# Optimization experiments

Measured on AMD Instinct MI355X. Metric: run time of the kernel, lower is better.

Reference implementation:

```python
import jax, jax.numpy as jnp
import numpy as np

B, S, E, H = 2, 2048, 1024, 16
D = E // H  # head_dim = 64
FE = 4      # forward_expansion
EPS = 1e-5


def layernorm(x, g, b):
    mu = jnp.mean(x, axis=-1, keepdims=True)
    var = jnp.var(x, axis=-1, keepdims=True)
    return (x - mu) * jax.lax.rsqrt(var + EPS) * g + b


def setup_inputs() -> dict:
    key = jax.random.key(0)
    ks = jax.random.split(key, 16)
    s = lambda d: 1.0 / np.sqrt(d)
    return {
        "queries": jax.random.normal(ks[0], (B, S, E), jnp.float32),
        "keys": jax.random.normal(ks[1], (B, S, E), jnp.float32),
        "values": jax.random.normal(ks[2], (B, S, E), jnp.float32),
        "mask": jnp.ones((B, 1, S, S), jnp.int32),  # ignored (faithful to source bug)
        "Wq": jax.random.normal(ks[3], (D, D), jnp.float32) * s(D),
        "Wk": jax.random.normal(ks[4], (D, D), jnp.float32) * s(D),
        "Wv": jax.random.normal(ks[5], (D, D), jnp.float32) * s(D),
        "Wfc": jax.random.normal(ks[6], (E, E), jnp.float32) * s(E),
        "bfc": jnp.zeros((E,), jnp.float32),
        "W1": jax.random.normal(ks[7], (FE * E, E), jnp.float32) * s(E),
        "b1": jnp.zeros((FE * E,), jnp.float32),
        "W2": jax.random.normal(ks[8], (E, FE * E), jnp.float32) * s(FE * E),
        "b2": jnp.zeros((E,), jnp.float32),
        "ln1_g": jnp.ones((E,), jnp.float32),
        "ln1_b": jnp.zeros((E,), jnp.float32),
        "ln2_g": jnp.ones((E,), jnp.float32),
        "ln2_b": jnp.zeros((E,), jnp.float32),
    }


def reference(queries, keys, values, mask, Wq, Wk, Wv, Wfc, bfc, W1, b1, W2, b2,
              ln1_g, ln1_b, ln2_g, ln2_b):
    # --- MHA ---
    q = queries.reshape(B, S, H, D) @ Wq.T  # [B,S,H,D]
    k = keys.reshape(B, S, H, D) @ Wk.T
    v = values.reshape(B, S, H, D) @ Wv.T
    scores = jnp.einsum('bqhd,bkhd->bhqk', q, k)
    # source: softmax(scores / S**(-1/2)) == scores * sqrt(S)  (faithful quirk)
    # mask is ignored: source masked_fill is non-inplace and discarded
    attn = jax.nn.softmax(scores * jnp.sqrt(jnp.float32(S)), axis=-1)
    out = jnp.einsum('bhqk,bkhd->bqhd', attn, v).reshape(B, S, E)
    att = out @ Wfc.T + bfc
    # --- residual + LN + FFN + LN (dropout p=0 -> identity) ---
    h = layernorm(att + queries, ln1_g, ln1_b)
    x = jax.nn.relu(h @ W1.T + b1) @ W2.T + b2
    return layernorm(x + h, ln2_g, ln2_b)
```

## Files before the change

kernel.cpp:

```cpp
#include <hip/hip_runtime.h>
#include <hip/hip_bf16.h>
#include <math.h>

#define B_ 2
#define S_ 2048
#define E_ 1024
#define H_ 16
#define D_ 64
#define TOK (B_*S_)
#define SCALE 45.254833995939045f
#define SCALE2 (45.254833995939045f * 1.44269504088896340f)

typedef __bf16 bf16x8 __attribute__((ext_vector_type(8)));
typedef float floatx4 __attribute__((ext_vector_type(4)));
struct b4s { __hip_bfloat16 x, y, z, w; };

typedef const __attribute__((address_space(1))) char ga_char;
typedef __attribute__((address_space(3))) char ls_char;

__device__ __forceinline__ void gload_lds16(const void* g, ls_char* l) {
  __builtin_amdgcn_global_load_lds((ga_char*)g, l, 16, 0, 0);
}

#if __has_builtin(__builtin_amdgcn_exp2f)
#define EXP2(x) __builtin_amdgcn_exp2f(x)
#else
#define EXP2(x) exp2f(x)
#endif

#define SWZ(arr, half, row, qpos) \
  (*(bf16x8*)&arr[half][row][(((qpos) ^ ((row) & 3)) * 8)])

__device__ __forceinline__ int fsw(int r) {
  return ((r >> 3) & 1) | ((((r >> 4) ^ (r >> 2)) & 1) << 1);
}
#define SWZ2(arr, half, row, qpos) \
  (*(bf16x8*)&arr[half][row][(((qpos) ^ fsw(row)) * 8)])

__global__ __launch_bounds__(256) void cast_all(
    const float* __restrict__ Wfc, const float* __restrict__ W1,
    const float* __restrict__ W2, __hip_bfloat16* __restrict__ Wfcb,
    __hip_bfloat16* __restrict__ W1b, __hip_bfloat16* __restrict__ W2b,
    const float* __restrict__ Wq, const float* __restrict__ Wk,
    const float* __restrict__ Wv, __hip_bfloat16* __restrict__ Whl) {
  const int i = blockIdx.x * 256 + threadIdx.x;
  if (i < 2359296) {
    const float* src; __hip_bfloat16* dst; int j;
    if (i < 262144)       { src = Wfc; dst = Wfcb; j = i; }
    else if (i < 1310720) { src = W1;  dst = W1b;  j = i - 262144; }
    else                  { src = W2;  dst = W2b;  j = i - 1310720; }
    float4 v = ((const float4*)src)[j];
    b4s o;
    o.x = __float2bfloat16(v.x); o.y = __float2bfloat16(v.y);
    o.z = __float2bfloat16(v.z); o.w = __float2bfloat16(v.w);
    *(b4s*)(dst + (size_t)j * 4) = o;
  } else if (i < 2362368) {
    const int idx = i - 2359296;
    const int m = idx >> 10;
    const int off = (idx & 1023) * 4;
    const float* W = (m == 0) ? Wq : (m == 1) ? Wk : Wv;
    float4 v = *(const float4*)(W + off);
    b4s hi, lo;
    hi.x = __float2bfloat16(v.x); lo.x = __float2bfloat16(v.x - __bfloat162float(hi.x));
    hi.y = __float2bfloat16(v.y); lo.y = __float2bfloat16(v.y - __bfloat162float(hi.y));
    hi.z = __float2bfloat16(v.z); lo.z = __float2bfloat16(v.z - __bfloat162float(hi.z));
    hi.w = __float2bfloat16(v.w); lo.w = __float2bfloat16(v.w - __bfloat162float(hi.w));
    *(b4s*)(Whl + (size_t)m * 8192 + off) = hi;
    *(b4s*)(Whl + (size_t)m * 8192 + 4096 + off) = lo;
  }
}

__global__ __launch_bounds__(256) void qkv_fused(
    const float* __restrict__ xq, const float* __restrict__ xk,
    const float* __restrict__ xv, const __hip_bfloat16* __restrict__ Whl,
    __hip_bfloat16* __restrict__ qhi, __hip_bfloat16* __restrict__ qlo,
    __hip_bfloat16* __restrict__ khi, __hip_bfloat16* __restrict__ klo,
    __hip_bfloat16* __restrict__ vt) {
  __shared__ __bf16 Xh[2][64][32], Xl[2][64][32];
  __shared__ __bf16 Vt[64][72];
  const int t = threadIdx.x, lane = t & 63, w = t >> 6;
  const int quad = lane >> 4, low = lane & 15;
  const int bh = blockIdx.y;
  const int b = bh >> 4, h = bh & 15;
  const int s0 = blockIdx.x * 64;
  const int sr = t >> 2;
  const int sc = (t & 3) * 16;
  const int scc = sc >> 5;
  const int p0 = (sc & 31) >> 3;

  for (int m = 0; m < 3; m++) {
    const float* xin = (m == 0) ? xq : (m == 1) ? xk : xv;
    const __hip_bfloat16* Wh = Whl + (size_t)m * 8192;
    const float sc_m = (m == 0) ? SCALE2 : 1.0f;

    __syncthreads();
    {
      const float* src = xin + ((size_t)(b * S_ + s0 + sr)) * E_ + h * 64 + sc;
      float4 f0 = *(const float4*)(src);
      float4 f1 = *(const float4*)(src + 4);
      float4 f2 = *(const float4*)(src + 8);
      float4 f3 = *(const float4*)(src + 12);
      float fv[16] = {f0.x, f0.y, f0.z, f0.w, f1.x, f1.y, f1.z, f1.w,
                      f2.x, f2.y, f2.z, f2.w, f3.x, f3.y, f3.z, f3.w};
      bf16x8 hi0, hi1, lo0, lo1;
      #pragma unroll
      for (int j = 0; j < 8; j++) {
        hi0[j] = (__bf16)fv[j];
        lo0[j] = (__bf16)(fv[j] - (float)hi0[j]);
        hi1[j] = (__bf16)fv[8 + j];
        lo1[j] = (__bf16)(fv[8 + j] - (float)hi1[j]);
      }
      SWZ(Xh, scc, sr, p0) = hi0;
      SWZ(Xh, scc, sr, p0 + 1) = hi1;
      SWZ(Xl, scc, sr, p0) = lo0;
      SWZ(Xl, scc, sr, p0 + 1) = lo1;
    }
    __syncthreads();

    bf16x8 ah[2], al[2];
    #pragma unroll
    for (int c = 0; c < 2; c++) {
      ah[c] = SWZ(Xh, c, w * 16 + low, quad);
      al[c] = SWZ(Xl, c, w * 16 + low, quad);
    }

    floatx4 acc[4];
    #pragma unroll
    for (int nn = 0; nn < 4; nn++) {
      floatx4 a = {};
      #pragma unroll
      for (int c = 0; c < 2; c++) {
        const __hip_bfloat16* wp = Wh + (nn * 16 + low) * 64 + c * 32 + quad * 8;
        bf16x8 wh_ = *(const bf16x8*)wp;
        bf16x8 wl_ = *(const bf16x8*)(wp + 4096);
        a = __builtin_amdgcn_mfma_f32_16x16x32_bf16(ah[c], wh_, a, 0, 0, 0);
        a = __builtin_amdgcn_mfma_f32_16x16x32_bf16(al[c], wh_, a, 0, 0, 0);
        a = __builtin_amdgcn_mfma_f32_16x16x32_bf16(ah[c], wl_, a, 0, 0, 0);
      }
      acc[nn] = a;
    }

    if (m < 2) {
      __hip_bfloat16* dh = (m == 0) ? qhi : khi;
      __hip_bfloat16* dl = (m == 0) ? qlo : klo;
      #pragma unroll
      for (int nn = 0; nn < 4; nn++) {
        #pragma unroll
        for (int i = 0; i < 4; i++) {
          const int s = s0 + w * 16 + quad * 4 + i;
          const int d = nn * 16 + low;
          const size_t adr = ((size_t)bh * S_ + s) * 64 + d;
          const float f = acc[nn][i] * sc_m;
          const __hip_bfloat16 hb = __float2bfloat16(f);
          dh[adr] = hb;
          dl[adr] = __float2bfloat16(f - __bfloat162float(hb));
        }
      }
    } else {
      #pragma unroll
      for (int nn = 0; nn < 4; nn++)
        #pragma unroll
        for (int i = 0; i < 4; i++)
          Vt[nn * 16 + low][w * 16 + quad * 4 + i] = (__bf16)acc[nn][i];
      __syncthreads();
      const int dr = t >> 2;
      const int scl = (t & 3) * 16;
      __hip_bfloat16* dst = vt + ((size_t)bh * 64 + dr) * S_ + s0 + scl;
      bf16x8 o0 = *(const bf16x8*)&Vt[dr][scl];
      bf16x8 o1 = *(const bf16x8*)&Vt[dr][scl + 8];
      *(bf16x8*)dst = o0;
      *(bf16x8*)(dst + 8) = o1;
    }
  }
}

__global__ __launch_bounds__(512, 4) void attn_mfma(
    const __hip_bfloat16* __restrict__ Qhi, const __hip_bfloat16* __restrict__ Qlo,
    const __hip_bfloat16* __restrict__ Khi, const __hip_bfloat16* __restrict__ Klo,
    const __hip_bfloat16* __restrict__ Vtg, __hip_bfloat16* __restrict__ ctx) {
  __shared__ __bf16 Kh[2][2][64][32], Kl[2][2][64][32], Vs[2][2][64][32];
  const int t = threadIdx.x, lane = t & 63, w = t >> 6;
  const int quad = lane >> 4, low = lane & 15;
  const int bh = blockIdx.x;
  const int qw = blockIdx.y * 128 + w * 16;

  const int sh = w >> 2;
  const int r0 = (w & 3) * 16;
  const int srow = r0 + (lane >> 2);
  const int sq = (lane & 3) ^ fsw(srow);
  const __hip_bfloat16* gK = Khi + ((size_t)bh * S_ + srow) * 64 + sh * 32 + sq * 8;
  const __hip_bfloat16* gL = Klo + ((size_t)bh * S_ + srow) * 64 + sh * 32 + sq * 8;
  const __hip_bfloat16* gV = Vtg + ((size_t)bh * 64 + srow) * S_ + sh * 32 + sq * 8;

  bf16x8 qh[2], ql[2];
  {
    const size_t qbase = ((size_t)bh * S_ + qw + low) * 64 + quad * 8;
    qh[0] = *(const bf16x8*)(Qhi + qbase);
    qh[1] = *(const bf16x8*)(Qhi + qbase + 32);
    ql[0] = *(const bf16x8*)(Qlo + qbase);
    ql[1] = *(const bf16x8*)(Qlo + qbase + 32);
  }

  floatx4 oacc[4] = {};
  float mrow = -3e38f, lrow = 0.f;

  gload_lds16(gK, (ls_char*)&Kh[0][sh][r0][0]);
  gload_lds16(gL, (ls_char*)&Kl[0][sh][r0][0]);
  gload_lds16(gV, (ls_char*)&Vs[0][sh][r0][0]);

  for (int kt = 0; kt < S_ / 64; kt++) {
    const int cur = kt & 1;
    __syncthreads();
    if (kt + 1 < S_ / 64) {
      gload_lds16(gK + (size_t)(kt + 1) * 4096, (ls_char*)&Kh[cur ^ 1][sh][r0][0]);
      gload_lds16(gL + (size_t)(kt + 1) * 4096, (ls_char*)&Kl[cur ^ 1][sh][r0][0]);
      gload_lds16(gV + (size_t)(kt + 1) * 64,   (ls_char*)&Vs[cur ^ 1][sh][r0][0]);
    }

    floatx4 sa[4];
    #pragma unroll
    for (int nn = 0; nn < 4; nn++) {
      const int prow = (nn & 1) * 32 + (nn >> 1) * 4 + (low >> 2) * 8 + (low & 3);
      bf16x8 kh0 = SWZ2(Kh[cur], 0, prow, quad);
      bf16x8 kh1 = SWZ2(Kh[cur], 1, prow, quad);
      bf16x8 kl0 = SWZ2(Kl[cur], 0, prow, quad);
      bf16x8 kl1 = SWZ2(Kl[cur], 1, prow, quad);
      floatx4 s = {};
      s = __builtin_amdgcn_mfma_f32_16x16x32_bf16(kh0, qh[0], s, 0, 0, 0);
      s = __builtin_amdgcn_mfma_f32_16x16x32_bf16(kh1, qh[1], s, 0, 0, 0);
      s = __builtin_amdgcn_mfma_f32_16x16x32_bf16(kl0, qh[0], s, 0, 0, 0);
      s = __builtin_amdgcn_mfma_f32_16x16x32_bf16(kl1, qh[1], s, 0, 0, 0);
      s = __builtin_amdgcn_mfma_f32_16x16x32_bf16(kh0, ql[0], s, 0, 0, 0);
      s = __builtin_amdgcn_mfma_f32_16x16x32_bf16(kh1, ql[1], s, 0, 0, 0);
      sa[nn] = s;
    }

    float rmax;
    {
      float m0 = fmaxf(fmaxf(sa[0][0], sa[0][1]), fmaxf(sa[0][2], sa[0][3]));
      float m1 = fmaxf(fmaxf(sa[1][0], sa[1][1]), fmaxf(sa[1][2], sa[1][3]));
      float m2 = fmaxf(fmaxf(sa[2][0], sa[2][1]), fmaxf(sa[2][2], sa[2][3]));
      float m3 = fmaxf(fmaxf(sa[3][0], sa[3][1]), fmaxf(sa[3][2], sa[3][3]));
      rmax = fmaxf(fmaxf(m0, m1), fmaxf(m2, m3));
      rmax = fmaxf(rmax, __shfl_xor(rmax, 16, 64));
      rmax = fmaxf(rmax, __shfl_xor(rmax, 32, 64));
    }
    if (__any(rmax > mrow)) {
      const float nm = fmaxf(mrow, rmax);
      const float al = EXP2(mrow - nm);
      mrow = nm;
      lrow *= al;
      #pragma unroll
      for (int dt = 0; dt < 4; dt++) {
        oacc[dt][0] *= al; oacc[dt][1] *= al;
        oacc[dt][2] *= al; oacc[dt][3] *= al;
      }
    }
    float p[4][4];
    float rs;
    {
      float r0_ = 0.f, r1_ = 0.f, r2_ = 0.f, r3_ = 0.f;
      #pragma unroll
      for (int i = 0; i < 4; i++) {
        p[0][i] = EXP2(sa[0][i] - mrow); r0_ += p[0][i];
        p[1][i] = EXP2(sa[1][i] - mrow); r1_ += p[1][i];
        p[2][i] = EXP2(sa[2][i] - mrow); r2_ += p[2][i];
        p[3][i] = EXP2(sa[3][i] - mrow); r3_ += p[3][i];
      }
      rs = (r0_ + r1_) + (r2_ + r3_);
      rs += __shfl_xor(rs, 16, 64);
      rs += __shfl_xor(rs, 32, 64);
    }
    lrow += rs;

    bf16x8 pb[2];
    #pragma unroll
    for (int kh2 = 0; kh2 < 2; kh2++) {
      bf16x8 v;
      v[0] = (__bf16)p[kh2][0]; v[1] = (__bf16)p[kh2][1];
      v[2] = (__bf16)p[kh2][2]; v[3] = (__bf16)p[kh2][3];
      v[4] = (__bf16)p[kh2 + 2][0]; v[5] = (__bf16)p[kh2 + 2][1];
      v[6] = (__bf16)p[kh2 + 2][2]; v[7] = (__bf16)p[kh2 + 2][3];
      pb[kh2] = v;
    }

    #pragma unroll
    for (int dt = 0; dt < 4; dt++) {
      bf16x8 vb0 = SWZ2(Vs[cur], 0, dt * 16 + low, quad);
      bf16x8 vb1 = SWZ2(Vs[cur], 1, dt * 16 + low, quad);
      oacc[dt] = __builtin_amdgcn_mfma_f32_16x16x32_bf16(vb0, pb[0], oacc[dt], 0, 0, 0);
      oacc[dt] = __builtin_amdgcn_mfma_f32_16x16x32_bf16(vb1, pb[1], oacc[dt], 0, 0, 0);
    }
  }

  const float inv = 1.0f / lrow;
  const int b = bh >> 4, h = bh & 15;
  const size_t base = ((size_t)(b * S_ + qw + low)) * E_ + h * 64 + quad * 4;
  #pragma unroll
  for (int dt = 0; dt < 4; dt++) {
    b4s o;
    o.x = __float2bfloat16(oacc[dt][0] * inv);
    o.y = __float2bfloat16(oacc[dt][1] * inv);
    o.z = __float2bfloat16(oacc[dt][2] * inv);
    o.w = __float2bfloat16(oacc[dt][3] * inv);
    *(b4s*)(ctx + base + dt * 16) = o;
  }
}

template <int RELU, int OUT_BF16, int PARTIAL>
__global__ __launch_bounds__(256) void gemm_mfma(
    const __hip_bfloat16* __restrict__ A, const __hip_bfloat16* __restrict__ Wt,
    const float* __restrict__ bias, void* __restrict__ C0, void* __restrict__ C1,
    int M, int N, int Kblk, int lda) {
  __shared__ __bf16 As[128][64];
  __shared__ __bf16 Bs[128][64];
  const int t = threadIdx.x;
  const int lane = t & 63;
  const int w = t >> 6;
  const int wr = w >> 1, wc = w & 1;
  const int m0 = blockIdx.y * 128, n0 = blockIdx.x * 128;
  void* Cout = (blockIdx.z == 0) ? C0 : C1;

  A += (size_t)blockIdx.z * Kblk;
  Wt += (size_t)blockIdx.z * Kblk;

  floatx4 acc[4][4] = {};
  const int srow = t >> 3;
  const int ssc = ((t & 7) ^ (srow & 7)) * 8;

  const __hip_bfloat16* gA = A + (size_t)(m0 + srow) * lda + ssc;
  const __hip_bfloat16* gB = Wt + (size_t)(n0 + srow) * lda + ssc;
  ls_char* lA = (ls_char*)&As[0][0] + w * 1024;
  ls_char* lB = (ls_char*)&Bs[0][0] + w * 1024;
  const size_t rstep = (size_t)32 * lda;

  for (int k0 = 0; k0 < Kblk; k0 += 64) {
    __syncthreads();
    gload_lds16(gA + k0,             lA);
    gload_lds16(gA + k0 + rstep,     lA + 4096);
    gload_lds16(gA + k0 + 2 * rstep, lA + 8192);
    gload_lds16(gA + k0 + 3 * rstep, lA + 12288);
    gload_lds16(gB + k0,             lB);
    gload_lds16(gB + k0 + rstep,     lB + 4096);
    gload_lds16(gB + k0 + 2 * rstep, lB + 8192);
    gload_lds16(gB + k0 + 3 * rstep, lB + 12288);
    __syncthreads();

    #pragma unroll
    for (int ks = 0; ks < 2; ks++) {
      bf16x8 af[4], bfr[4];
      #pragma unroll
      for (int i = 0; i < 4; i++) {
        const int ra = wr * 64 + i * 16 + (lane & 15);
        const int ca = (((lane >> 4) + ks * 4) ^ (ra & 7)) * 8;
        af[i] = *(const bf16x8*)&As[ra][ca];
        const int rb = wc * 64 + i * 16 + (lane & 15);
        const int cb = (((lane >> 4) + ks * 4) ^ (rb & 7)) * 8;
        bfr[i] = *(const bf16x8*)&Bs[rb][cb];
      }
      #pragma unroll
      for (int mi = 0; mi < 4; mi++)
        #pragma unroll
        for (int ni = 0; ni < 4; ni++)
          acc[mi][ni] = __builtin_amdgcn_mfma_f32_16x16x32_bf16(
              af[mi], bfr[ni], acc[mi][ni], 0, 0, 0);
    }
  }

  const int cil = lane & 15;
  const int quad = lane >> 4;
  #pragma unroll
  for (int ni = 0; ni < 4; ni++) {
    const int col = n0 + wc * 64 + ni * 16 + cil;
    const float bb = PARTIAL ? 0.f : bias[col];
    #pragma unroll
    for (int mi = 0; mi < 4; mi++) {
      const int row = m0 + wr * 64 + mi * 16 + quad * 4;
      #pragma unroll
      for (int i = 0; i < 4; i++) {
        if (PARTIAL) {
          ((float*)Cout)[(size_t)(row + i) * N + col] = acc[mi][ni][i];
        } else {
          float vv = acc[mi][ni][i] + bb;
          if (RELU) vv = fmaxf(vv, 0.f);
          if (OUT_BF16)
            ((__hip_bfloat16*)Cout)[(size_t)(row + i) * N + col] = __float2bfloat16(vv);
          else
            ((float*)Cout)[(size_t)(row + i) * N + col] = vv;
        }
      }
    }
  }
}

template <int EMIT_BF16>
__global__ __launch_bounds__(256) void add_ln(
    const float* __restrict__ a0, const float* __restrict__ a1,
    const float* __restrict__ r, const float* __restrict__ bias,
    const float* __restrict__ g, const float* __restrict__ bt,
    float* __restrict__ out, __hip_bfloat16* __restrict__ outb) {
  __shared__ float red[16];
  const int tok = blockIdx.x, t = threadIdx.x;
  float4 av = ((const float4*)(a0 + (size_t)tok * E_))[t];
  float4 a2 = ((const float4*)(a1 + (size_t)tok * E_))[t];
  float4 rv = ((const float4*)(r + (size_t)tok * E_))[t];
  float4 cv = ((const float4*)bias)[t];
  float4 x;
  x.x = av.x + a2.x + rv.x + cv.x; x.y = av.y + a2.y + rv.y + cv.y;
  x.z = av.z + a2.z + rv.z + cv.z; x.w = av.w + a2.w + rv.w + cv.w;
  float sum = x.x + x.y + x.z + x.w;
  float ssq = x.x * x.x + x.y * x.y + x.z * x.z + x.w * x.w;
  #pragma unroll
  for (int off = 32; off >= 1; off >>= 1) {
    sum += __shfl_down(sum, off, 64);
    ssq += __shfl_down(ssq, off, 64);
  }
  const int wave = t >> 6;
  if ((t & 63) == 0) { red[wave] = sum; red[4 + wave] = ssq; }
  __syncthreads();
  if (t == 0) {
    float s = red[0] + red[1] + red[2] + red[3];
    float qq = red[4] + red[5] + red[6] + red[7];
    float mu = s * (1.0f / E_);
    red[8] = mu;
    red[9] = qq * (1.0f / E_) - mu * mu;
  }
  __syncthreads();
  const float mu = red[8];
  const float inv = rsqrtf(red[9] + 1e-5f);
  float4 gv = ((const float4*)g)[t];
  float4 bv = ((const float4*)bt)[t];
  float4 o;
  o.x = (x.x - mu) * inv * gv.x + bv.x;
  o.y = (x.y - mu) * inv * gv.y + bv.y;
  o.z = (x.z - mu) * inv * gv.z + bv.z;
  o.w = (x.w - mu) * inv * gv.w + bv.w;
  ((float4*)(out + (size_t)tok * E_))[t] = o;
  if (EMIT_BF16) {
    b4s ob;
    ob.x = __float2bfloat16(o.x); ob.y = __float2bfloat16(o.y);
    ob.z = __float2bfloat16(o.z); ob.w = __float2bfloat16(o.w);
    *(b4s*)(outb + (size_t)tok * E_ + t * 4) = ob;
  }
}

extern "C" void kernel_launch(void* const* d_in, const int* in_sizes, int n_in,
                              void* d_out, int out_size, void* d_ws, size_t ws_size,
                              hipStream_t stream) {
  const float* queries = (const float*)d_in[0];
  const float* keys    = (const float*)d_in[1];
  const float* values  = (const float*)d_in[2];
  const float* Wq  = (const float*)d_in[4];
  const float* Wk  = (const float*)d_in[5];
  const float* Wv  = (const float*)d_in[6];
  const float* Wfc = (const float*)d_in[7];
  const float* bfc = (const float*)d_in[8];
  const float* W1  = (const float*)d_in[9];
  const float* b1  = (const float*)d_in[10];
  const float* W2  = (const float*)d_in[11];
  const float* b2  = (const float*)d_in[12];
  const float* ln1_g = (const float*)d_in[13];
  const float* ln1_b = (const float*)d_in[14];
  const float* ln2_g = (const float*)d_in[15];
  const float* ln2_b = (const float*)d_in[16];

  const size_t M1 = 1048576;
  float* ws = (float*)d_ws;
  float* P0  = ws;
  float* P1  = ws + 4 * M1;
  float* Hf  = ws + 8 * M1;
  __hip_bfloat16* bb = (__hip_bfloat16*)(ws + 12 * M1);
  __hip_bfloat16* CTXb = bb;
  __hip_bfloat16* Hb   = bb + 4 * M1;
  __hip_bfloat16* Wfcb = bb + 8 * M1;
  __hip_bfloat16* W1b  = bb + 9 * M1;
  __hip_bfloat16* W2b  = bb + 13 * M1;
  __hip_bfloat16* Qhi  = bb + 17 * M1;
  __hip_bfloat16* Qlo  = bb + 21 * M1;
  __hip_bfloat16* Khi  = bb + 25 * M1;
  __hip_bfloat16* Klo  = bb + 29 * M1;
  __hip_bfloat16* Vtb  = bb + 33 * M1;
  __hip_bfloat16* FF1b = bb + 17 * M1;
  __hip_bfloat16* Whlb = bb + 37 * M1;
  float* out = (float*)d_out;

  cast_all<<<9228, 256, 0, stream>>>(Wfc, W1, W2, Wfcb, W1b, W2b,
                                     Wq, Wk, Wv, Whlb);

  qkv_fused<<<dim3(S_ / 64, B_ * H_), 256, 0, stream>>>(
      queries, keys, values, Whlb, Qhi, Qlo, Khi, Klo, Vtb);
  attn_mfma<<<dim3(B_ * H_, S_ / 128), 512, 0, stream>>>(
      Qhi, Qlo, Khi, Klo, Vtb, CTXb);
  gemm_mfma<0, 0, 1><<<dim3(E_ / 128, TOK / 128, 2), 256, 0, stream>>>(
      CTXb, Wfcb, nullptr, P0, P1, TOK, E_, 512, E_);
  add_ln<1><<<TOK, 256, 0, stream>>>(P0, P1, queries, bfc, ln1_g, ln1_b, Hf, Hb);
  gemm_mfma<1, 1, 0><<<dim3(4 * E_ / 128, TOK / 128, 1), 256, 0, stream>>>(
      Hb, W1b, b1, FF1b, FF1b, TOK, 4 * E_, E_, E_);
  gemm_mfma<0, 0, 1><<<dim3(E_ / 128, TOK / 128, 2), 256, 0, stream>>>(
      FF1b, W2b, nullptr, P0, P1, TOK, E_, 2048, 4 * E_);
  add_ln<0><<<TOK, 256, 0, stream>>>(P0, P1, Hf, b2, ln2_g, ln2_b, out, nullptr);
}
```

Measured before the change: 397.2 us.

## Process two query tiles per wave in attention to reuse K/V LDS reads

The attention kernel now runs 256 threads per block, with each wave handling two 16-row query tiles instead of one. Each K/V fragment read from LDS therefore feeds two sets of MFMAs, and the interleaved independent accumulators give more instruction-level parallelism. Staging changes so each wave loads both 32-column halves, and the LDS swizzle reverts to the simpler row&3 XOR pattern. In exchange, register pressure roughly doubles, launch bounds drop to 2 blocks per SM, and the simpler swizzle may bring back bank conflicts.

```diff
diff --git a/kernel.cpp b/kernel.cpp
--- a/kernel.cpp
+++ b/kernel.cpp
@@ -8,7 +8,6 @@
 #define H_ 16
 #define D_ 64
 #define TOK (B_*S_)
-#define SCALE 45.254833995939045f
 #define SCALE2 (45.254833995939045f * 1.44269504088896340f)
 
 typedef __bf16 bf16x8 __attribute__((ext_vector_type(8)));
@@ -30,12 +29,6 @@
 
 #define SWZ(arr, half, row, qpos) \
   (*(bf16x8*)&arr[half][row][(((qpos) ^ ((row) & 3)) * 8)])
-
-__device__ __forceinline__ int fsw(int r) {
-  return ((r >> 3) & 1) | ((((r >> 4) ^ (r >> 2)) & 1) << 1);
-}
-#define SWZ2(arr, half, row, qpos) \
-  (*(bf16x8*)&arr[half][row][(((qpos) ^ fsw(row)) * 8)])
 
 __global__ __launch_bounds__(256) void cast_all(
     const float* __restrict__ Wfc, const float* __restrict__ W1,
@@ -174,7 +167,57 @@
   }
 }
 
-__global__ __launch_bounds__(512, 4) void attn_mfma(
+__device__ __forceinline__ void softmax_update(
+    const floatx4* sa, floatx4* oacc, float& mrow, float& lrow, bf16x8* pb) {
+  float rmax;
+  {
+    float m0 = fmaxf(fmaxf(sa[0][0], sa[0][1]), fmaxf(sa[0][2], sa[0][3]));
+    float m1 = fmaxf(fmaxf(sa[1][0], sa[1][1]), fmaxf(sa[1][2], sa[1][3]));
+    float m2 = fmaxf(fmaxf(sa[2][0], sa[2][1]), fmaxf(sa[2][2], sa[2][3]));
+    float m3 = fmaxf(fmaxf(sa[3][0], sa[3][1]), fmaxf(sa[3][2], sa[3][3]));
+    rmax = fmaxf(fmaxf(m0, m1), fmaxf(m2, m3));
+    rmax = fmaxf(rmax, __shfl_xor(rmax, 16, 64));
+    rmax = fmaxf(rmax, __shfl_xor(rmax, 32, 64));
+  }
+  if (__any(rmax > mrow)) {
+    const float nm = fmaxf(mrow, rmax);
+    const float al = EXP2(mrow - nm);
+    mrow = nm;
+    lrow *= al;
+    #pragma unroll
+    for (int dt = 0; dt < 4; dt++) {
+      oacc[dt][0] *= al; oacc[dt][1] *= al;
+      oacc[dt][2] *= al; oacc[dt][3] *= al;
+    }
+  }
+  float p[4][4];
+  float rs;
+  {
+    float r0_ = 0.f, r1_ = 0.f, r2_ = 0.f, r3_ = 0.f;
+    #pragma unroll
+    for (int i = 0; i < 4; i++) {
+      p[0][i] = EXP2(sa[0][i] - mrow); r0_ += p[0][i];
+      p[1][i] = EXP2(sa[1][i] - mrow); r1_ += p[1][i];
+      p[2][i] = EXP2(sa[2][i] - mrow); r2_ += p[2][i];
+      p[3][i] = EXP2(sa[3][i] - mrow); r3_ += p[3][i];
+    }
+    rs = (r0_ + r1_) + (r2_ + r3_);
+    rs += __shfl_xor(rs, 16, 64);
+    rs += __shfl_xor(rs, 32, 64);
+  }
+  lrow += rs;
+  #pragma unroll
+  for (int kh2 = 0; kh2 < 2; kh2++) {
+    bf16x8 v;
+    v[0] = (__bf16)p[kh2][0]; v[1] = (__bf16)p[kh2][1];
+    v[2] = (__bf16)p[kh2][2]; v[3] = (__bf16)p[kh2][3];
+    v[4] = (__bf16)p[kh2 + 2][0]; v[5] = (__bf16)p[kh2 + 2][1];
+    v[6] = (__bf16)p[kh2 + 2][2]; v[7] = (__bf16)p[kh2 + 2][3];
+    pb[kh2] = v;
+  }
+}
+
+__global__ __launch_bounds__(256, 2) void attn_mfma(
     const __hip_bfloat16* __restrict__ Qhi, const __hip_bfloat16* __restrict__ Qlo,
     const __hip_bfloat16* __restrict__ Khi, const __hip_bfloat16* __restrict__ Klo,
     const __hip_bfloat16* __restrict__ Vtg, __hip_bfloat16* __restrict__ ctx) {
@@ -182,128 +225,118 @@
   const int t = threadIdx.x, lane = t & 63, w = t >> 6;
   const int quad = lane >> 4, low = lane & 15;
   const int bh = blockIdx.x;
-  const int qw = blockIdx.y * 128 + w * 16;
-
-  const int sh = w >> 2;
-  const int r0 = (w & 3) * 16;
+  const int qw0 = blockIdx.y * 128 + w * 16;
+  const int qw1 = qw0 + 64;
+
+  const int r0 = w * 16;
   const int srow = r0 + (lane >> 2);
-  const int sq = (lane & 3) ^ fsw(srow);
-  const __hip_bfloat16* gK = Khi + ((size_t)bh * S_ + srow) * 64 + sh * 32 + sq * 8;
-  const __hip_bfloat16* gL = Klo + ((size_t)bh * S_ + srow) * 64 + sh * 32 + sq * 8;
-  const __hip_bfloat16* gV = Vtg + ((size_t)bh * 64 + srow) * S_ + sh * 32 + sq * 8;
-
-  bf16x8 qh[2], ql[2];
+  const int sq = (lane & 3) ^ (srow & 3);
+  const __hip_bfloat16* gK = Khi + ((size_t)bh * S_ + srow) * 64 + sq * 8;
+  const __hip_bfloat16* gL = Klo + ((size_t)bh * S_ + srow) * 64 + sq * 8;
+  const __hip_bfloat16* gV = Vtg + ((size_t)bh * 64 + srow) * S_ + sq * 8;
+
+#define STAGE(buf, kt) do {                                        \
+    const size_t ko = (size_t)(kt) * 4096;                         \
+    const size_t vo = (size_t)(kt) * 64;                           \
+    gload_lds16(gK + ko,      (ls_char*)&Kh[buf][0][r0][0]);       \
+    gload_lds16(gK + ko + 32, (ls_char*)&Kh[buf][1][r0][0]);       \
+    gload_lds16(gL + ko,      (ls_char*)&Kl[buf][0][r0][0]);       \
+    gload_lds16(gL + ko + 32, (ls_char*)&Kl[buf][1][r0][0]);       \
+    gload_lds16(gV + vo,      (ls_char*)&Vs[buf][0][r0][0]);       \
+    gload_lds16(gV + vo + 32, (ls_char*)&Vs[buf][1][r0][0]);       \
+  } while (0)
+
+  bf16x8 qh0[2], ql0[2], qh1[2], ql1[2];
   {
-    const size_t qbase = ((size_t)bh * S_ + qw + low) * 64 + quad * 8;
-    qh[0] = *(const bf16x8*)(Qhi + qbase);
-    qh[1] = *(const bf16x8*)(Qhi + qbase + 32);
-    ql[0] = *(const bf16x8*)(Qlo + qbase);
-    ql[1] = *(const bf16x8*)(Qlo + qbase + 32);
-  }
-
-  floatx4 oacc[4] = {};
-  float mrow = -3e38f, lrow = 0.f;
-
-  gload_lds16(gK, (ls_char*)&Kh[0][sh][r0][0]);
-  gload_lds16(gL, (ls_char*)&Kl[0][sh][r0][0]);
-  gload_lds16(gV, (ls_char*)&Vs[0][sh][r0][0]);
+    const size_t qb0 = ((size_t)bh * S_ + qw0 + low) * 64 + quad * 8;
+    const size_t qb1 = ((size_t)bh * S_ + qw1 + low) * 64 + quad * 8;
+    qh0[0] = *(const bf16x8*)(Qhi + qb0);
+    qh0[1] = *(const bf16x8*)(Qhi + qb0 + 32);
+    ql0[0] = *(const bf16x8*)(Qlo + qb0);
+    ql0[1] = *(const bf16x8*)(Qlo + qb0 + 32);
+    qh1[0] = *(const bf16x8*)(Qhi + qb1);
+    qh1[1] = *(const bf16x8*)(Qhi + qb1 + 32);
+    ql1[0] = *(const bf16x8*)(Qlo + qb1);
+    ql1[1] = *(const bf16x8*)(Qlo + qb1 + 32);
+  }
+
+  floatx4 oacc0[4] = {}, oacc1[4] = {};
+  float mrow0 = -3e38f, lrow0 = 0.f, mrow1 = -3e38f, lrow1 = 0.f;
+
+  STAGE(0, 0);
 
   for (int kt = 0; kt < S_ / 64; kt++) {
     const int cur = kt & 1;
     __syncthreads();
-    if (kt + 1 < S_ / 64) {
-      gload_lds16(gK + (size_t)(kt + 1) * 4096, (ls_char*)&Kh[cur ^ 1][sh][r0][0]);
-      gload_lds16(gL + (size_t)(kt + 1) * 4096, (ls_char*)&Kl[cur ^ 1][sh][r0][0]);
-      gload_lds16(gV + (size_t)(kt + 1) * 64,   (ls_char*)&Vs[cur ^ 1][sh][r0][0]);
-    }
-
-    floatx4 sa[4];
+    if (kt + 1 < S_ / 64) STAGE(cur ^ 1, kt + 1);
+
+    floatx4 sa0[4], sa1[4];
     #pragma unroll
     for (int nn = 0; nn < 4; nn++) {
       const int prow = (nn & 1) * 32 + (nn >> 1) * 4 + (low >> 2) * 8 + (low & 3);
-      bf16x8 kh0 = SWZ2(Kh[cur], 0, prow, quad);
-      bf16x8 kh1 = SWZ2(Kh[cur], 1, prow, quad);
-      bf16x8 kl0 = SWZ2(Kl[cur], 0, prow, quad);
-      bf16x8 kl1 = SWZ2(Kl[cur], 1, prow, quad);
-      floatx4 s = {};
-      s = __builtin_amdgcn_mfma_f32_16x16x32_bf16(kh0, qh[0], s, 0, 0, 0);
-      s = __builtin_amdgcn_mfma_f32_16x16x32_bf16(kh1, qh[1], s, 0, 0, 0);
-      s = __builtin_amdgcn_mfma_f32_16x16x32_bf16(kl0, qh[0], s, 0, 0, 0);
-      s = __builtin_amdgcn_mfma_f32_16x16x32_bf16(kl1, qh[1], s, 0, 0, 0);
-      s = __builtin_amdgcn_mfma_f32_16x16x32_bf16(kh0, ql[0], s, 0, 0, 0);
-      s = __builtin_amdgcn_mfma_f32_16x16x32_bf16(kh1, ql[1], s, 0, 0, 0);
-      sa[nn] = s;
-    }
-
-    float rmax;
-    {
-      float m0 = fmaxf(fmaxf(sa[0][0], sa[0][1]), fmaxf(sa[0][2], sa[0][3]));
-      float m1 = fmaxf(fmaxf(sa[1][0], sa[1][1]), fmaxf(sa[1][2], sa[1][3]));
-      float m2 = fmaxf(fmaxf(sa[2][0], sa[2][1]), fmaxf(sa[2][2], sa[2][3]));
-      float m3 = fmaxf(fmaxf(sa[3][0], sa[3][1]), fmaxf(sa[3][2], sa[3][3]));
-      rmax = fmaxf(fmaxf(m0, m1), fmaxf(m2, m3));
-      rmax = fmaxf(rmax, __shfl_xor(rmax, 16, 64));
-      rmax = fmaxf(rmax, __shfl_xor(rmax, 32, 64));
-    }
-    if (__any(rmax > mrow)) {
-      const float nm = fmaxf(mrow, rmax);
-      const float al = EXP2(mrow - nm);
-      mrow = nm;
-      lrow *= al;
-      #pragma unroll
-      for (int dt = 0; dt < 4; dt++) {
-        oacc[dt][0] *= al; oacc[dt][1] *= al;
-        oacc[dt][2] *= al; oacc[dt][3] *= al;
-      }
-    }
-    float p[4][4];
-    float rs;
-    {
-      float r0_ = 0.f, r1_ = 0.f, r2_ = 0.f, r3_ = 0.f;
-      #pragma unroll
-      for (int i = 0; i < 4; i++) {
-        p[0][i] = EXP2(sa[0][i] - mrow); r0_ += p[0][i];
-        p[1][i] = EXP2(sa[1][i] - mrow); r1_ += p[1][i];
-        p[2][i] = EXP2(sa[2][i] - mrow); r2_ += p[2][i];
-        p[3][i] = EXP2(sa[3][i] - mrow); r3_ += p[3][i];
-      }
-      rs = (r0_ + r1_) + (r2_ + r3_);
-      rs += __shfl_xor(rs, 16, 64);
-      rs += __shfl_xor(rs, 32, 64);
-    }
-    lrow += rs;
-
-    bf16x8 pb[2];
-    #pragma unroll
-    for (int kh2 = 0; kh2 < 2; kh2++) {
-      bf16x8 v;
-      v[0] = (__bf16)p[kh2][0]; v[1] = (__bf16)p[kh2][1];
-      v[2] = (__bf16)p[kh2][2]; v[3] = (__bf16)p[kh2][3];
-      v[4] = (__bf16)p[kh2 + 2][0]; v[5] = (__bf16)p[kh2 + 2][1];
-      v[6] = (__bf16)p[kh2 + 2][2]; v[7] = (__bf16)p[kh2 + 2][3];
-      pb[kh2] = v;
-    }
+      bf16x8 kh0 = SWZ(Kh[cur], 0, prow, quad);
+      bf16x8 kh1 = SWZ(Kh[cur], 1, prow, quad);
+      bf16x8 kl0 = SWZ(Kl[cur], 0, prow, quad);
+      bf16x8 kl1 = SWZ(Kl[cur], 1, prow, quad);
+      floatx4 s0 = {}, s1 = {};
+      s0 = __builtin_amdgcn_mfma_f32_16x16x32_bf16(kh0, qh0[0], s0, 0, 0, 0);
+      s1 = __builtin_amdgcn_mfma_f32_16x16x32_bf16(kh0, qh1[0], s1, 0, 0, 0);
+      s0 = __builtin_amdgcn_mfma_f32_16x16x32_bf16(kh1, qh0[1], s0, 0, 0, 0);
+      s1 = __builtin_amdgcn_mfma_f32_16x16x32_bf16(kh1, qh1[1], s1, 0, 0, 0);
+      s0 = __builtin_amdgcn_mfma_f32_16x16x32_bf16(kl0, qh0[0], s0, 0, 0, 0);
+      s1 = __builtin_amdgcn_mfma_f32_16x16x32_bf16(kl0, qh1[0], s1, 0, 0, 0);
+      s0 = __builtin_amdgcn_mfma_f32_16x16x32_bf16(kl1, qh0[1], s0, 0, 0, 0);
+      s1 = __builtin_amdgcn_mfma_f32_16x16x32_bf16(kl1, qh1[1], s1, 0, 0, 0);
+      s0 = __builtin_amdgcn_mfma_f32_16x16x32_bf16(kh0, ql0[0], s0, 0, 0, 0);
+      s1 = __builtin_amdgcn_mfma_f32_16x16x32_bf16(kh0, ql1[0], s1, 0, 0, 0);
+      s0 = __builtin_amdgcn_mfma_f32_16x16x32_bf16(kh1, ql0[1], s0, 0, 0, 0);
+      s1 = __builtin_amdgcn_mfma_f32_16x16x32_bf16(kh1, ql1[1], s1, 0, 0, 0);
+      sa0[nn] = s0;
+      sa1[nn] = s1;
+    }
+
+    bf16x8 pb0[2], pb1[2];
+    softmax_update(sa0, oacc0, mrow0, lrow0, pb0);
+    softmax_update(sa1, oacc1, mrow1, lrow1, pb1);
 
     #pragma unroll
     for (int dt = 0; dt < 4; dt++) {
-      bf16x8 vb0 = SWZ2(Vs[cur], 0, dt * 16 + low, quad);
-      bf16x8 vb1 = SWZ2(Vs[cur], 1, dt * 16 + low, quad);
-      oacc[dt] = __builtin_amdgcn_mfma_f32_16x16x32_bf16(vb0, pb[0], oacc[dt], 0, 0, 0);
-      oacc[dt] = __builtin_amdgcn_mfma_f32_16x16x32_bf16(vb1, pb[1], oacc[dt], 0, 0, 0);
-    }
-  }
-
-  const float inv = 1.0f / lrow;
+      bf16x8 vb0 = SWZ(Vs[cur], 0, dt * 16 + low, quad);
+      bf16x8 vb1 = SWZ(Vs[cur], 1, dt * 16 + low, quad);
+      oacc0[dt] = __builtin_amdgcn_mfma_f32_16x16x32_bf16(vb0, pb0[0], oacc0[dt], 0, 0, 0);
+      oacc1[dt] = __builtin_amdgcn_mfma_f32_16x16x32_bf16(vb0, pb1[0], oacc1[dt], 0, 0, 0);
+      oacc0[dt] = __builtin_amdgcn_mfma_f32_16x16x32_bf16(vb1, pb0[1], oacc0[dt], 0, 0, 0);
+      oacc1[dt] = __builtin_amdgcn_mfma_f32_16x16x32_bf16(vb1, pb1[1], oacc1[dt], 0, 0, 0);
+    }
+  }
+#undef STAGE
+
   const int b = bh >> 4, h = bh & 15;
-  const size_t base = ((size_t)(b * S_ + qw + low)) * E_ + h * 64 + quad * 4;
-  #pragma unroll
-  for (int dt = 0; dt < 4; dt++) {
-    b4s o;
-    o.x = __float2bfloat16(oacc[dt][0] * inv);
-    o.y = __float2bfloat16(oacc[dt][1] * inv);
-    o.z = __float2bfloat16(oacc[dt][2] * inv);
-    o.w = __float2bfloat16(oacc[dt][3] * inv);
-    *(b4s*)(ctx + base + dt * 16) = o;
+  {
+    const float inv = 1.0f / lrow0;
+    const size_t base = ((size_t)(b * S_ + qw0 + low)) * E_ + h * 64 + quad * 4;
+    #pragma unroll
+    for (int dt = 0; dt < 4; dt++) {
+      b4s o;
+      o.x = __float2bfloat16(oacc0[dt][0] * inv);
+      o.y = __float2bfloat16(oacc0[dt][1] * inv);
+      o.z = __float2bfloat16(oacc0[dt][2] * inv);
+      o.w = __float2bfloat16(oacc0[dt][3] * inv);
+      *(b4s*)(ctx + base + dt * 16) = o;
+    }
+  }
+  {
+    const float inv = 1.0f / lrow1;
+    const size_t base = ((size_t)(b * S_ + qw1 + low)) * E_ + h * 64 + quad * 4;
+    #pragma unroll
+    for (int dt = 0; dt < 4; dt++) {
+      b4s o;
+      o.x = __float2bfloat16(oacc1[dt][0] * inv);
+      o.y = __float2bfloat16(oacc1[dt][1] * inv);
+      o.z = __float2bfloat16(oacc1[dt][2] * inv);
+      o.w = __float2bfloat16(oacc1[dt][3] * inv);
+      *(b4s*)(ctx + base + dt * 16) = o;
+    }
   }
 }
 
@@ -489,7 +522,7 @@
 
   qkv_fused<<<dim3(S_ / 64, B_ * H_), 256, 0, stream>>>(
       queries, keys, values, Whlb, Qhi, Qlo, Khi, Klo, Vtb);
-  attn_mfma<<<dim3(B_ * H_, S_ / 128), 512, 0, stream>>>(
+  attn_mfma<<<dim3(B_ * H_, S_ / 128), 256, 0, stream>>>(
       Qhi, Qlo, Khi, Klo, Vtb, CTXb);
   gemm_mfma<0, 0, 1><<<dim3(E_ / 128, TOK / 128, 2), 256, 0, stream>>>(
       CTXb, Wfcb, nullptr, P0, P1, TOK, E_, 512, E_);
```

Result: no change. 391.9 us (-1.3%).
